# Optimization experiments

Hardware: AMD Instinct MI355X
Metric: run time of the kernel (lower is better)

The kernel has to match this reference:

```python
import jax, jax.numpy as jnp
import numpy as np


def setup_inputs() -> dict:
    key = jax.random.key(0)
    x = jax.random.normal(key, (8192, 4096), dtype=jnp.float32)
    return {"x": x, "p": 64}


def reference(x, p):
    # training-mode path: find top-p indices per row (descending sort, first p)
    # and overwrite those positions with -1000. mask = ones, so mask*x == x.
    _, idx = jax.lax.top_k(x, p)                      # [B, p] int32
    rows = jnp.arange(x.shape[0])[:, None]            # [B, 1]
    out = x.at[rows, idx].set(jnp.float32(-1000.0))
    return out
```

## Files before the change

### kernel.cpp

```cpp
#include <hip/hip_runtime.h>
#include <stdint.h>

#define COLS 4096
#define TPB  256
#define F4PT 4
#define CAP  128
#define NEGV (-1000.0f)

__device__ __forceinline__ uint32_t f2key(float f) {
    uint32_t u = __float_as_uint(f);
    return u ^ (uint32_t)(((int32_t)u >> 31) | (int32_t)0x80000000);
}
__device__ __forceinline__ float key2f(uint32_t k) {
    uint32_t u = (k & 0x80000000u) ? (k ^ 0x80000000u) : ~k;
    return __uint_as_float(u);
}

template <int PER>
__device__ __forceinline__ void find_bin(const uint32_t* hist, int t, int lane, int wave,
                                         uint32_t rem, volatile uint32_t* s_wsum,
                                         volatile uint32_t* s_dig, volatile uint32_t* s_rem) {
    const int base = t * PER;
    uint32_t own[PER]; uint32_t L = 0;
#pragma unroll
    for (int i = 0; i < PER; ++i) { own[i] = hist[base + i]; L += own[i]; }
    uint32_t inc = L;
#pragma unroll
    for (int d = 1; d < 64; d <<= 1) {
        uint32_t tmp = (uint32_t)__shfl_down((int)inc, d, 64);
        if (lane + d < 64) inc += tmp;
    }
    if (lane == 0) s_wsum[wave] = inc;
    __syncthreads();
    uint32_t U = inc - L;
#pragma unroll
    for (int w = 1; w < 4; ++w) if (wave + w < 4) U += s_wsum[wave + w];
    uint32_t acc = U;
#pragma unroll
    for (int i = PER - 1; i >= 0; --i) {
        uint32_t h = own[i];
        if (h && acc < rem && rem <= acc + h) { *s_dig = (uint32_t)(base + i); *s_rem = rem - acc; }
        acc += h;
    }
    __syncthreads();
}

extern "C" __global__ __launch_bounds__(TPB, 8)
void intent_dropout_kernel(const float* __restrict__ x,
                           const int* __restrict__ pp,
                           float* __restrict__ out) {
    __shared__ uint32_t s_h1[2048];
    __shared__ uint32_t s_ck[CAP], s_ci[CAP];
    __shared__ uint32_t s_grpmax[64];
    __shared__ uint32_t s_wsum[4];
    __shared__ uint32_t s_Ckey, s_dig, s_remv, s_cnt, s_cnt2, s_Tkey, s_cutIdx, s_pbtie;

    const int row  = blockIdx.x;
    const int t    = threadIdx.x;
    const int lane = t & 63;
    const int wave = t >> 6;
    const uint32_t P = (uint32_t)pp[0];

    const float4* xr   = (const float4*)(x + (size_t)row * COLS);
    float4*       orow = (float4*)(out + (size_t)row * COLS);

#pragma unroll
    for (int i = 0; i < 8; ++i) s_h1[t + TPB * i] = 0u;
    if (t == 0) { s_cnt = 0u; s_cnt2 = 0u; }

    uint32_t keys[16];
#pragma unroll
    for (int j = 0; j < F4PT; ++j) {
        float4 v = xr[t + TPB * j];
        keys[4*j+0] = f2key(v.x); keys[4*j+1] = f2key(v.y);
        keys[4*j+2] = f2key(v.z); keys[4*j+3] = f2key(v.w);
        uint32_t m = max(max(keys[4*j], keys[4*j+1]), max(keys[4*j+2], keys[4*j+3]));
#pragma unroll
        for (int d = 1; d < 16; d <<= 1) m = max(m, (uint32_t)__shfl_xor((int)m, d, 64));
        if ((lane & 15) == 0) s_grpmax[(t >> 4) + 16 * j] = m;
    }
    __syncthreads();
    if (t < 64) {
        uint32_t g = s_grpmax[t];
#pragma unroll
        for (int d = 1; d < 64; d <<= 1) g = min(g, (uint32_t)__shfl_xor((int)g, d, 64));
        if (t == 0) s_Ckey = g;
    }
    __syncthreads();
    const uint32_t Ckey = s_Ckey;

#pragma unroll
    for (int i = 0; i < 16; ++i)
        if (keys[i] >= Ckey) atomicAdd(&s_h1[keys[i] >> 21], 1u);
    __syncthreads();
    find_bin<8>(s_h1, t, lane, wave, P, s_wsum, &s_dig, &s_remv);
    const uint32_t d1 = s_dig, rem1 = s_remv;

#pragma unroll
    for (int j = 0; j < F4PT; ++j) {
#pragma unroll
        for (int c = 0; c < 4; ++c) {
            uint32_t k = keys[4*j+c];
            if (k >= Ckey && (k >> 21) == d1) {
                uint32_t s = atomicAdd(&s_cnt, 1u);
                if (s < CAP) { s_ck[s] = k; s_ci[s] = (uint32_t)(4*(t + TPB*j) + c); }
            }
        }
    }
    __syncthreads();
    const uint32_t cnt = s_cnt;

    if (cnt <= CAP) {
        if (t < 64) {
            uint32_t ka = 0, ia = 0, kb = 0, ib = 0;
            const bool ha = (uint32_t)t < cnt, hb = (uint32_t)(t + 64) < cnt;
            if (ha) { ka = s_ck[t];      ia = s_ci[t]; }
            if (hb) { kb = s_ck[t + 64]; ib = s_ci[t + 64]; }
            uint32_t ra = 0, rb = 0;
            for (uint32_t e = 0; e < cnt; ++e) {
                uint32_t ke = s_ck[e], ie = s_ci[e];
                ra += (uint32_t)((ke > ka) || (ke == ka && ie < ia));
                rb += (uint32_t)((ke > kb) || (ke == kb && ie < ib));
            }
            if (ha && ra == rem1 - 1u) { s_Tkey = ka; s_cutIdx = ia; }
            if (hb && rb == rem1 - 1u) { s_Tkey = kb; s_cutIdx = ib; }
        }
        __syncthreads();
    } else {
#pragma unroll
        for (int i = 0; i < 8; ++i) s_h1[t + TPB * i] = 0u;
        __syncthreads();
#pragma unroll
        for (int i = 0; i < 16; ++i) {
            uint32_t k = keys[i];
            if (k >= Ckey && (k >> 21) == d1) atomicAdd(&s_h1[(k >> 10) & 0x7FFu], 1u);
        }
        __syncthreads();
        find_bin<8>(s_h1, t, lane, wave, rem1, s_wsum, &s_dig, &s_remv);
        const uint32_t d2 = s_dig, rem2 = s_remv;
        const uint32_t pre21 = (d1 << 11) | d2;
#pragma unroll
        for (int j = 0; j < F4PT; ++j) {
#pragma unroll
            for (int c = 0; c < 4; ++c) {
                uint32_t k = keys[4*j+c];
                if (k >= Ckey && (k >> 10) == pre21) {
                    uint32_t s = atomicAdd(&s_cnt2, 1u);
                    if (s < CAP) { s_ck[s] = k; s_ci[s] = (uint32_t)(4*(t + TPB*j) + c); }
                }
            }
        }
        __syncthreads();
        const uint32_t cnt2 = s_cnt2;
        if (cnt2 <= CAP) {
            if (t < 64) {
                uint32_t ka = 0, ia = 0, kb = 0, ib = 0;
                const bool ha = (uint32_t)t < cnt2, hb = (uint32_t)(t + 64) < cnt2;
                if (ha) { ka = s_ck[t];      ia = s_ci[t]; }
                if (hb) { kb = s_ck[t + 64]; ib = s_ci[t + 64]; }
                uint32_t ra = 0, rb = 0;
                for (uint32_t e = 0; e < cnt2; ++e) {
                    uint32_t ke = s_ck[e], ie = s_ci[e];
                    ra += (uint32_t)((ke > ka) || (ke == ka && ie < ia));
                    rb += (uint32_t)((ke > kb) || (ke == kb && ie < ib));
                }
                if (ha && ra == rem2 - 1u) { s_Tkey = ka; s_cutIdx = ia; }
                if (hb && rb == rem2 - 1u) { s_Tkey = kb; s_cutIdx = ib; }
            }
            __syncthreads();
        } else {
#pragma unroll
            for (int i = 0; i < 8; ++i) s_h1[t + TPB * i] = 0u;
            __syncthreads();
#pragma unroll
            for (int i = 0; i < 16; ++i) {
                uint32_t k = keys[i];
                if (k >= Ckey && (k >> 10) == pre21) atomicAdd(&s_h1[k & 0x3FFu], 1u);
            }
            __syncthreads();
            find_bin<4>(s_h1, t, lane, wave, rem2, s_wsum, &s_dig, &s_remv);
            const uint32_t Tk  = (pre21 << 10) | s_dig;
            const uint32_t keq = s_remv;
#pragma unroll
            for (int i = 0; i < 8; ++i) s_h1[t + TPB * i] = 0u;
            __syncthreads();
#pragma unroll
            for (int j = 0; j < F4PT; ++j)
#pragma unroll
                for (int c = 0; c < 4; ++c)
                    if (keys[4*j+c] == Tk)
                        atomicAdd(&s_h1[2047u - ((uint32_t)(4*(t + TPB*j) + c) >> 1)], 1u);
            __syncthreads();
            find_bin<8>(s_h1, t, lane, wave, keq, s_wsum, &s_dig, &s_remv);
            const uint32_t br = s_dig, remv = s_remv;
            const uint32_t pairBase = 2u * (2047u - br);
            {
                const uint32_t f = pairBase >> 2;
                if ((uint32_t)t == (f & (uint32_t)(TPB - 1))) {
                    const uint32_t jj = f >> 8, cc = pairBase & 3u;
                    s_pbtie = (uint32_t)(keys[4*jj + cc] == Tk);
                }
            }
            __syncthreads();
            if (t == 0) {
                const uint32_t cp = s_h1[br];
                uint32_t cut;
                if (cp >= 2u) cut = (remv == 1u) ? pairBase : pairBase + 1u;
                else          cut = s_pbtie ? pairBase : pairBase + 1u;
                s_Tkey = Tk; s_cutIdx = cut;
            }
            __syncthreads();
        }
    }

    const uint32_t Tkey = s_Tkey, cutIdx = s_cutIdx;
#pragma unroll
    for (int j = 0; j < F4PT; ++j) {
        float4 o;
        float* c4 = (float*)&o;
#pragma unroll
        for (int c = 0; c < 4; ++c) {
            const uint32_t k   = keys[4*j+c];
            const uint32_t idx = (uint32_t)(4*(t + TPB*j) + c);
            const bool kill = (k > Tkey) || (k == Tkey && idx <= cutIdx);
            c4[c] = kill ? NEGV : key2f(k);
        }
        orow[t + TPB * j] = o;
    }
}

extern "C" void kernel_launch(void* const* d_in, const int* in_sizes, int n_in,
                              void* d_out, int out_size, void* d_ws, size_t ws_size,
                              hipStream_t stream) {
    const float* x   = (const float*)d_in[0];
    const int*   pp  = (const int*)d_in[1];
    float*       out = (float*)d_out;
    int rows = in_sizes[0] / COLS;
    hipLaunchKernelGGL(intent_dropout_kernel, dim3(rows), dim3(TPB), 0, stream,
                       x, pp, out);
}
```

Baseline: 242.8 us.

## Process two rows per block with packed dual-row histogram and shared radix select

Each block now handles two rows. Both rows' first-level radix histograms are packed into one shared array using 16-bit halves, so a single prefix-scan pass finds the bucket for both rows. The group-max prefilter (Ckey) is removed, so every element goes into the histogram. The small-candidate rank selects for the two rows run on separate waves, and the rare refinement path is moved into a cold helper function. This is meant to amortize barriers and scan work across rows and to put more loads in flight per thread. In exchange it doubles register use, lowers launch bounds to 4, halves the grid size, and relies on per-row counts staying under 65536, which holds since each row has 4096 elements.

```diff
diff --git a/kernel.cpp b/kernel.cpp
--- a/kernel.cpp
+++ b/kernel.cpp
@@ -3,7 +3,6 @@
 
 #define COLS 4096
 #define TPB  256
-#define F4PT 4
 #define CAP  128
 #define NEGV (-1000.0f)
 
@@ -16,14 +15,13 @@
     return __uint_as_float(u);
 }
 
-template <int PER>
-__device__ __forceinline__ void find_bin(const uint32_t* hist, int t, int lane, int wave,
-                                         uint32_t rem, volatile uint32_t* s_wsum,
-                                         volatile uint32_t* s_dig, volatile uint32_t* s_rem) {
-    const int base = t * PER;
-    uint32_t own[PER]; uint32_t L = 0;
-#pragma unroll
-    for (int i = 0; i < PER; ++i) { own[i] = hist[base + i]; L += own[i]; }
+__device__ __forceinline__ void find_bin8(const uint32_t* hist, int t, int lane, int wave,
+                                          uint32_t rem, uint32_t* s_wsum,
+                                          uint32_t* s_dig, uint32_t* s_rem) {
+    const int base = t * 8;
+    uint32_t own[8]; uint32_t L = 0;
+#pragma unroll
+    for (int i = 0; i < 8; ++i) { own[i] = hist[base + i]; L += own[i]; }
     uint32_t inc = L;
 #pragma unroll
     for (int d = 1; d < 64; d <<= 1) {
@@ -37,7 +35,7 @@
     for (int w = 1; w < 4; ++w) if (wave + w < 4) U += s_wsum[wave + w];
     uint32_t acc = U;
 #pragma unroll
-    for (int i = PER - 1; i >= 0; --i) {
+    for (int i = 7; i >= 0; --i) {
         uint32_t h = own[i];
         if (h && acc < rem && rem <= acc + h) { *s_dig = (uint32_t)(base + i); *s_rem = rem - acc; }
         acc += h;
@@ -45,187 +43,246 @@
     __syncthreads();
 }
 
-extern "C" __global__ __launch_bounds__(TPB, 8)
+__device__ __forceinline__ void rank_select(const uint32_t* ck, const uint32_t* ci,
+                                            uint32_t cnt, uint32_t rem, int lane,
+                                            uint32_t* tkey, uint32_t* cut) {
+    uint32_t ka = 0, ia = 0, kb = 0, ib = 0;
+    const bool ha = (uint32_t)lane < cnt, hb = (uint32_t)(lane + 64) < cnt;
+    if (ha) { ka = ck[lane];      ia = ci[lane]; }
+    if (hb) { kb = ck[lane + 64]; ib = ci[lane + 64]; }
+    uint32_t ra = 0, rb = 0;
+    for (uint32_t e = 0; e < cnt; ++e) {
+        uint32_t ke = ck[e], ie = ci[e];
+        ra += (uint32_t)((ke > ka) || (ke == ka && ie < ia));
+        rb += (uint32_t)((ke > kb) || (ke == kb && ie < ib));
+    }
+    if (ha && ra == rem - 1u) { *tkey = ka; *cut = ia; }
+    if (hb && rb == rem - 1u) { *tkey = kb; *cut = ib; }
+}
+
+__device__ void solve_row_cold(const uint32_t (&k)[16], uint32_t d1, uint32_t rem1,
+                               uint32_t* s_h, uint32_t* s_ck, uint32_t* s_ci,
+                               uint32_t* s_wsum, uint32_t* s_dig, uint32_t* s_remv,
+                               uint32_t* s_cnt2, uint32_t* s_pbtie,
+                               uint32_t* tkey, uint32_t* cut,
+                               int t, int lane, int wave) {
+#pragma unroll
+    for (int i = 0; i < 8; ++i) s_h[t + TPB * i] = 0u;
+    if (t == 0) *s_cnt2 = 0u;
+    __syncthreads();
+#pragma unroll
+    for (int i = 0; i < 16; ++i)
+        if ((k[i] >> 21) == d1) atomicAdd(&s_h[(k[i] >> 10) & 0x7FFu], 1u);
+    __syncthreads();
+    find_bin8(s_h, t, lane, wave, rem1, s_wsum, s_dig, s_remv);
+    const uint32_t d2 = *s_dig, rem2 = *s_remv;
+    const uint32_t pre21 = (d1 << 11) | d2;
+#pragma unroll
+    for (int j = 0; j < 4; ++j)
+#pragma unroll
+        for (int c = 0; c < 4; ++c) {
+            uint32_t kk = k[4 * j + c];
+            if ((kk >> 10) == pre21) {
+                uint32_t s = atomicAdd(s_cnt2, 1u);
+                if (s < CAP) { s_ck[s] = kk; s_ci[s] = (uint32_t)(4 * (t + TPB * j) + c); }
+            }
+        }
+    __syncthreads();
+    const uint32_t cnt2 = *s_cnt2;
+    if (cnt2 <= CAP) {
+        if (wave == 0) rank_select(s_ck, s_ci, cnt2, rem2, lane, tkey, cut);
+        __syncthreads();
+        return;
+    }
+#pragma unroll
+    for (int i = 0; i < 8; ++i) s_h[t + TPB * i] = 0u;
+    __syncthreads();
+#pragma unroll
+    for (int i = 0; i < 16; ++i)
+        if ((k[i] >> 10) == pre21) atomicAdd(&s_h[k[i] & 0x3FFu], 1u);
+    __syncthreads();
+    find_bin8(s_h, t, lane, wave, rem2, s_wsum, s_dig, s_remv);
+    const uint32_t Tk = (pre21 << 10) | *s_dig;
+    const uint32_t keq = *s_remv;
+#pragma unroll
+    for (int i = 0; i < 8; ++i) s_h[t + TPB * i] = 0u;
+    __syncthreads();
+#pragma unroll
+    for (int j = 0; j < 4; ++j)
+#pragma unroll
+        for (int c = 0; c < 4; ++c)
+            if (k[4 * j + c] == Tk)
+                atomicAdd(&s_h[2047u - ((uint32_t)(4 * (t + TPB * j) + c) >> 1)], 1u);
+    __syncthreads();
+    find_bin8(s_h, t, lane, wave, keq, s_wsum, s_dig, s_remv);
+    const uint32_t br = *s_dig, remv = *s_remv;
+    const uint32_t pairBase = 2u * (2047u - br);
+    {
+        const uint32_t f = pairBase >> 2;
+        if ((uint32_t)t == (f & (uint32_t)(TPB - 1))) {
+            const int sel = (int)(4u * (f >> 8) + (pairBase & 3u));
+            uint32_t kv = 0;
+#pragma unroll
+            for (int q = 0; q < 16; ++q) if (q == sel) kv = k[q];
+            *s_pbtie = (uint32_t)(kv == Tk);
+        }
+    }
+    __syncthreads();
+    if (t == 0) {
+        const uint32_t cp = s_h[br];
+        uint32_t cu;
+        if (cp >= 2u) cu = (remv == 1u) ? pairBase : pairBase + 1u;
+        else          cu = (*s_pbtie) ? pairBase : pairBase + 1u;
+        *tkey = Tk; *cut = cu;
+    }
+    __syncthreads();
+}
+
+extern "C" __global__ __launch_bounds__(TPB, 4)
 void intent_dropout_kernel(const float* __restrict__ x,
                            const int* __restrict__ pp,
                            float* __restrict__ out) {
-    __shared__ uint32_t s_h1[2048];
-    __shared__ uint32_t s_ck[CAP], s_ci[CAP];
-    __shared__ uint32_t s_grpmax[64];
+    __shared__ uint32_t s_h[2048];
+    __shared__ uint32_t s_ck0[CAP], s_ci0[CAP];
+    __shared__ uint32_t s_ck1[CAP], s_ci1[CAP];
     __shared__ uint32_t s_wsum[4];
-    __shared__ uint32_t s_Ckey, s_dig, s_remv, s_cnt, s_cnt2, s_Tkey, s_cutIdx, s_pbtie;
-
-    const int row  = blockIdx.x;
-    const int t    = threadIdx.x;
-    const int lane = t & 63;
-    const int wave = t >> 6;
+    __shared__ uint32_t s_cnt0, s_cnt1, s_cnt2, s_pbtie;
+    __shared__ uint32_t s_d[2], s_r[2];
+    __shared__ uint32_t s_Tk[2], s_cut[2];
+    __shared__ uint32_t s_dig, s_remv;
+
+    const int t = threadIdx.x, lane = t & 63, wave = t >> 6;
     const uint32_t P = (uint32_t)pp[0];
-
-    const float4* xr   = (const float4*)(x + (size_t)row * COLS);
-    float4*       orow = (float4*)(out + (size_t)row * COLS);
-
-#pragma unroll
-    for (int i = 0; i < 8; ++i) s_h1[t + TPB * i] = 0u;
-    if (t == 0) { s_cnt = 0u; s_cnt2 = 0u; }
-
-    uint32_t keys[16];
-#pragma unroll
-    for (int j = 0; j < F4PT; ++j) {
-        float4 v = xr[t + TPB * j];
-        keys[4*j+0] = f2key(v.x); keys[4*j+1] = f2key(v.y);
-        keys[4*j+2] = f2key(v.z); keys[4*j+3] = f2key(v.w);
-        uint32_t m = max(max(keys[4*j], keys[4*j+1]), max(keys[4*j+2], keys[4*j+3]));
-#pragma unroll
-        for (int d = 1; d < 16; d <<= 1) m = max(m, (uint32_t)__shfl_xor((int)m, d, 64));
-        if ((lane & 15) == 0) s_grpmax[(t >> 4) + 16 * j] = m;
-    }
-    __syncthreads();
-    if (t < 64) {
-        uint32_t g = s_grpmax[t];
-#pragma unroll
-        for (int d = 1; d < 64; d <<= 1) g = min(g, (uint32_t)__shfl_xor((int)g, d, 64));
-        if (t == 0) s_Ckey = g;
-    }
-    __syncthreads();
-    const uint32_t Ckey = s_Ckey;
-
-#pragma unroll
-    for (int i = 0; i < 16; ++i)
-        if (keys[i] >= Ckey) atomicAdd(&s_h1[keys[i] >> 21], 1u);
-    __syncthreads();
-    find_bin<8>(s_h1, t, lane, wave, P, s_wsum, &s_dig, &s_remv);
-    const uint32_t d1 = s_dig, rem1 = s_remv;
-
-#pragma unroll
-    for (int j = 0; j < F4PT; ++j) {
+    const int row0 = blockIdx.x * 2;
+
+    const float4* x0 = (const float4*)(x + (size_t)row0 * COLS);
+    const float4* x1 = (const float4*)(x + (size_t)(row0 + 1) * COLS);
+    float4* o0 = (float4*)(out + (size_t)row0 * COLS);
+    float4* o1 = (float4*)(out + (size_t)(row0 + 1) * COLS);
+
+#pragma unroll
+    for (int i = 0; i < 8; ++i) s_h[t + TPB * i] = 0u;
+    if (t == 0) { s_cnt0 = 0u; s_cnt1 = 0u; }
+
+    uint32_t k0[16], k1[16];
+#pragma unroll
+    for (int j = 0; j < 4; ++j) {
+        float4 v = x0[t + TPB * j];
+        k0[4*j+0] = f2key(v.x); k0[4*j+1] = f2key(v.y);
+        k0[4*j+2] = f2key(v.z); k0[4*j+3] = f2key(v.w);
+    }
+#pragma unroll
+    for (int j = 0; j < 4; ++j) {
+        float4 v = x1[t + TPB * j];
+        k1[4*j+0] = f2key(v.x); k1[4*j+1] = f2key(v.y);
+        k1[4*j+2] = f2key(v.z); k1[4*j+3] = f2key(v.w);
+    }
+    __syncthreads();
+
+#pragma unroll
+    for (int i = 0; i < 16; ++i) atomicAdd(&s_h[k0[i] >> 21], 1u);
+#pragma unroll
+    for (int i = 0; i < 16; ++i) atomicAdd(&s_h[k1[i] >> 21], 0x10000u);
+    __syncthreads();
+
+    {
+        const int base = t * 8;
+        uint32_t own[8]; uint32_t L = 0;
+#pragma unroll
+        for (int i = 0; i < 8; ++i) { own[i] = s_h[base + i]; L += own[i]; }
+        uint32_t inc = L;
+#pragma unroll
+        for (int d = 1; d < 64; d <<= 1) {
+            uint32_t tmp = (uint32_t)__shfl_down((int)inc, d, 64);
+            if (lane + d < 64) inc += tmp;
+        }
+        if (lane == 0) s_wsum[wave] = inc;
+        __syncthreads();
+        uint32_t U = inc - L;
+#pragma unroll
+        for (int w = 1; w < 4; ++w) if (wave + w < 4) U += s_wsum[wave + w];
+        uint32_t a0 = U & 0xFFFFu, a1 = U >> 16;
+#pragma unroll
+        for (int i = 7; i >= 0; --i) {
+            uint32_t h0 = own[i] & 0xFFFFu, h1 = own[i] >> 16;
+            if (h0 && a0 < P && P <= a0 + h0) { s_d[0] = (uint32_t)(base + i); s_r[0] = P - a0; }
+            if (h1 && a1 < P && P <= a1 + h1) { s_d[1] = (uint32_t)(base + i); s_r[1] = P - a1; }
+            a0 += h0; a1 += h1;
+        }
+        __syncthreads();
+    }
+    const uint32_t d1_0 = s_d[0], r1_0 = s_r[0];
+    const uint32_t d1_1 = s_d[1], r1_1 = s_r[1];
+
+#pragma unroll
+    for (int j = 0; j < 4; ++j)
 #pragma unroll
         for (int c = 0; c < 4; ++c) {
-            uint32_t k = keys[4*j+c];
-            if (k >= Ckey && (k >> 21) == d1) {
-                uint32_t s = atomicAdd(&s_cnt, 1u);
-                if (s < CAP) { s_ck[s] = k; s_ci[s] = (uint32_t)(4*(t + TPB*j) + c); }
-            }
-        }
-    }
-    __syncthreads();
-    const uint32_t cnt = s_cnt;
-
-    if (cnt <= CAP) {
-        if (t < 64) {
-            uint32_t ka = 0, ia = 0, kb = 0, ib = 0;
-            const bool ha = (uint32_t)t < cnt, hb = (uint32_t)(t + 64) < cnt;
-            if (ha) { ka = s_ck[t];      ia = s_ci[t]; }
-            if (hb) { kb = s_ck[t + 64]; ib = s_ci[t + 64]; }
-            uint32_t ra = 0, rb = 0;
-            for (uint32_t e = 0; e < cnt; ++e) {
-                uint32_t ke = s_ck[e], ie = s_ci[e];
-                ra += (uint32_t)((ke > ka) || (ke == ka && ie < ia));
-                rb += (uint32_t)((ke > kb) || (ke == kb && ie < ib));
-            }
-            if (ha && ra == rem1 - 1u) { s_Tkey = ka; s_cutIdx = ia; }
-            if (hb && rb == rem1 - 1u) { s_Tkey = kb; s_cutIdx = ib; }
-        }
+            uint32_t kk = k0[4*j+c];
+            if ((kk >> 21) == d1_0) {
+                uint32_t s = atomicAdd(&s_cnt0, 1u);
+                if (s < CAP) { s_ck0[s] = kk; s_ci0[s] = (uint32_t)(4*(t + TPB*j) + c); }
+            }
+        }
+#pragma unroll
+    for (int j = 0; j < 4; ++j)
+#pragma unroll
+        for (int c = 0; c < 4; ++c) {
+            uint32_t kk = k1[4*j+c];
+            if ((kk >> 21) == d1_1) {
+                uint32_t s = atomicAdd(&s_cnt1, 1u);
+                if (s < CAP) { s_ck1[s] = kk; s_ci1[s] = (uint32_t)(4*(t + TPB*j) + c); }
+            }
+        }
+    __syncthreads();
+    const uint32_t c0 = s_cnt0, c1 = s_cnt1;
+
+    if (c0 <= CAP && c1 <= CAP) {
+        if (wave == 0)      rank_select(s_ck0, s_ci0, c0, r1_0, lane, &s_Tk[0], &s_cut[0]);
+        else if (wave == 1) rank_select(s_ck1, s_ci1, c1, r1_1, lane, &s_Tk[1], &s_cut[1]);
         __syncthreads();
     } else {
-#pragma unroll
-        for (int i = 0; i < 8; ++i) s_h1[t + TPB * i] = 0u;
-        __syncthreads();
-#pragma unroll
-        for (int i = 0; i < 16; ++i) {
-            uint32_t k = keys[i];
-            if (k >= Ckey && (k >> 21) == d1) atomicAdd(&s_h1[(k >> 10) & 0x7FFu], 1u);
-        }
-        __syncthreads();
-        find_bin<8>(s_h1, t, lane, wave, rem1, s_wsum, &s_dig, &s_remv);
-        const uint32_t d2 = s_dig, rem2 = s_remv;
-        const uint32_t pre21 = (d1 << 11) | d2;
-#pragma unroll
-        for (int j = 0; j < F4PT; ++j) {
-#pragma unroll
-            for (int c = 0; c < 4; ++c) {
-                uint32_t k = keys[4*j+c];
-                if (k >= Ckey && (k >> 10) == pre21) {
-                    uint32_t s = atomicAdd(&s_cnt2, 1u);
-                    if (s < CAP) { s_ck[s] = k; s_ci[s] = (uint32_t)(4*(t + TPB*j) + c); }
-                }
-            }
-        }
-        __syncthreads();
-        const uint32_t cnt2 = s_cnt2;
-        if (cnt2 <= CAP) {
-            if (t < 64) {
-                uint32_t ka = 0, ia = 0, kb = 0, ib = 0;
-                const bool ha = (uint32_t)t < cnt2, hb = (uint32_t)(t + 64) < cnt2;
-                if (ha) { ka = s_ck[t];      ia = s_ci[t]; }
-                if (hb) { kb = s_ck[t + 64]; ib = s_ci[t + 64]; }
-                uint32_t ra = 0, rb = 0;
-                for (uint32_t e = 0; e < cnt2; ++e) {
-                    uint32_t ke = s_ck[e], ie = s_ci[e];
-                    ra += (uint32_t)((ke > ka) || (ke == ka && ie < ia));
-                    rb += (uint32_t)((ke > kb) || (ke == kb && ie < ib));
-                }
-                if (ha && ra == rem2 - 1u) { s_Tkey = ka; s_cutIdx = ia; }
-                if (hb && rb == rem2 - 1u) { s_Tkey = kb; s_cutIdx = ib; }
-            }
+        if (c0 <= CAP) {
+            if (wave == 0) rank_select(s_ck0, s_ci0, c0, r1_0, lane, &s_Tk[0], &s_cut[0]);
             __syncthreads();
         } else {
-#pragma unroll
-            for (int i = 0; i < 8; ++i) s_h1[t + TPB * i] = 0u;
+            solve_row_cold(k0, d1_0, r1_0, s_h, s_ck0, s_ci0, s_wsum, &s_dig, &s_remv,
+                           &s_cnt2, &s_pbtie, &s_Tk[0], &s_cut[0], t, lane, wave);
+        }
+        if (c1 <= CAP) {
+            if (wave == 0) rank_select(s_ck1, s_ci1, c1, r1_1, lane, &s_Tk[1], &s_cut[1]);
             __syncthreads();
-#pragma unroll
-            for (int i = 0; i < 16; ++i) {
-                uint32_t k = keys[i];
-                if (k >= Ckey && (k >> 10) == pre21) atomicAdd(&s_h1[k & 0x3FFu], 1u);
-            }
-            __syncthreads();
-            find_bin<4>(s_h1, t, lane, wave, rem2, s_wsum, &s_dig, &s_remv);
-            const uint32_t Tk  = (pre21 << 10) | s_dig;
-            const uint32_t keq = s_remv;
-#pragma unroll
-            for (int i = 0; i < 8; ++i) s_h1[t + TPB * i] = 0u;
-            __syncthreads();
-#pragma unroll
-            for (int j = 0; j < F4PT; ++j)
-#pragma unroll
-                for (int c = 0; c < 4; ++c)
-                    if (keys[4*j+c] == Tk)
-                        atomicAdd(&s_h1[2047u - ((uint32_t)(4*(t + TPB*j) + c) >> 1)], 1u);
-            __syncthreads();
-            find_bin<8>(s_h1, t, lane, wave, keq, s_wsum, &s_dig, &s_remv);
-            const uint32_t br = s_dig, remv = s_remv;
-            const uint32_t pairBase = 2u * (2047u - br);
-            {
-                const uint32_t f = pairBase >> 2;
-                if ((uint32_t)t == (f & (uint32_t)(TPB - 1))) {
-                    const uint32_t jj = f >> 8, cc = pairBase & 3u;
-                    s_pbtie = (uint32_t)(keys[4*jj + cc] == Tk);
-                }
-            }
-            __syncthreads();
-            if (t == 0) {
-                const uint32_t cp = s_h1[br];
-                uint32_t cut;
-                if (cp >= 2u) cut = (remv == 1u) ? pairBase : pairBase + 1u;
-                else          cut = s_pbtie ? pairBase : pairBase + 1u;
-                s_Tkey = Tk; s_cutIdx = cut;
-            }
-            __syncthreads();
-        }
-    }
-
-    const uint32_t Tkey = s_Tkey, cutIdx = s_cutIdx;
-#pragma unroll
-    for (int j = 0; j < F4PT; ++j) {
-        float4 o;
-        float* c4 = (float*)&o;
-#pragma unroll
-        for (int c = 0; c < 4; ++c) {
-            const uint32_t k   = keys[4*j+c];
-            const uint32_t idx = (uint32_t)(4*(t + TPB*j) + c);
-            const bool kill = (k > Tkey) || (k == Tkey && idx <= cutIdx);
-            c4[c] = kill ? NEGV : key2f(k);
-        }
-        orow[t + TPB * j] = o;
+        } else {
+            solve_row_cold(k1, d1_1, r1_1, s_h, s_ck1, s_ci1, s_wsum, &s_dig, &s_remv,
+                           &s_cnt2, &s_pbtie, &s_Tk[1], &s_cut[1], t, lane, wave);
+        }
+    }
+
+    {
+        const uint32_t T0 = s_Tk[0], X0 = s_cut[0];
+#pragma unroll
+        for (int j = 0; j < 4; ++j) {
+            float4 o; float* c4 = (float*)&o;
+#pragma unroll
+            for (int c = 0; c < 4; ++c) {
+                uint32_t kk = k0[4*j+c];
+                uint32_t idx = (uint32_t)(4*(t + TPB*j) + c);
+                c4[c] = ((kk > T0) || (kk == T0 && idx <= X0)) ? NEGV : key2f(kk);
+            }
+            o0[t + TPB * j] = o;
+        }
+        const uint32_t T1 = s_Tk[1], X1 = s_cut[1];
+#pragma unroll
+        for (int j = 0; j < 4; ++j) {
+            float4 o; float* c4 = (float*)&o;
+#pragma unroll
+            for (int c = 0; c < 4; ++c) {
+                uint32_t kk = k1[4*j+c];
+                uint32_t idx = (uint32_t)(4*(t + TPB*j) + c);
+                c4[c] = ((kk > T1) || (kk == T1 && idx <= X1)) ? NEGV : key2f(kk);
+            }
+            o1[t + TPB * j] = o;
+        }
     }
 }
 
@@ -236,6 +293,6 @@
     const int*   pp  = (const int*)d_in[1];
     float*       out = (float*)d_out;
     int rows = in_sizes[0] / COLS;
-    hipLaunchKernelGGL(intent_dropout_kernel, dim3(rows), dim3(TPB), 0, stream,
+    hipLaunchKernelGGL(intent_dropout_kernel, dim3(rows / 2), dim3(TPB), 0, stream,
                        x, pp, out);
 }
```

New measurement: 236.8 us. 1.03x faster.
